# Performance work log

Hardware: AMD Instinct MI355X
Metric: run time of the kernel (lower is better)

## Reference

```python
import jax, jax.numpy as jnp
import numpy as np
import math

N_HEAD = 16

def setup_inputs() -> dict:
    key = jax.random.key(0)
    k1, k2, k3, k4, k5 = jax.random.split(key, 5)
    B, S, D = 2, 2048, 1024
    return {
        "hidden_states": jax.random.normal(k1, (B, S, D), dtype=jnp.float32),
        "c_attn_w": jax.random.normal(k2, (D, 3 * D), dtype=jnp.float32) * 0.02,
        "c_attn_b": jax.random.normal(k3, (3 * D,), dtype=jnp.float32) * 0.02,
        "c_proj_w": jax.random.normal(k4, (D, D), dtype=jnp.float32) * 0.02,
        "c_proj_b": jax.random.normal(k5, (D,), dtype=jnp.float32) * 0.02,
    }

def reference(hidden_states, c_attn_w, c_attn_b, c_proj_w, c_proj_b):
    B, S, D = hidden_states.shape
    H = N_HEAD
    hd = D // H
    # GPT-2 Conv1D: x @ W + b, W is [in, out]
    qkv = hidden_states @ c_attn_w + c_attn_b            # [B,S,3D]
    q, k, v = jnp.split(qkv, 3, axis=-1)                 # each [B,S,D]
    # sparsify_q/k/v_fn are identity hooks in this config
    def to_heads(x):
        return x.reshape(B, S, H, hd).transpose(0, 2, 1, 3)  # [B,H,S,hd]
    q, k, v = to_heads(q), to_heads(k), to_heads(v)
    scores = jnp.einsum("bhqd,bhkd->bhqk", q, k) / math.sqrt(hd)  # [B,H,S,S]
    causal = jnp.triu(jnp.ones((S, S), dtype=bool), k=1)
    scores = jnp.where(causal, jnp.finfo(scores.dtype).min, scores)
    attn = jax.nn.softmax(scores, axis=-1)
    out = jnp.einsum("bhqk,bhkd->bhqd", attn, v)         # [B,H,S,hd]
    out = out.transpose(0, 2, 1, 3).reshape(B, S, D)
    return out @ c_proj_w + c_proj_b
```

## Files before the change

### kernel.cpp

```cpp
#include <hip/hip_runtime.h>
#include <stdint.h>


#define B_   2
#define S_   2048
#define D_   1024
#define H_   16
#define HD_  64

typedef __bf16 bf16x8 __attribute__((ext_vector_type(8)));
typedef float  f32x4  __attribute__((ext_vector_type(4)));
typedef float  f32x16 __attribute__((ext_vector_type(16)));
typedef uint32_t u32x4 __attribute__((ext_vector_type(4)));

__device__ __forceinline__ float b2f(uint16_t u) {
    union { uint32_t i; float f; } x; x.i = ((uint32_t)u) << 16; return x.f;
}
__device__ __forceinline__ uint16_t f2b(float f) {
    uint32_t x = __builtin_bit_cast(uint32_t, f);
    x += 0x7fffu + ((x >> 16) & 1u);
    return (uint16_t)(x >> 16);
}
__device__ __forceinline__ float sq(float f) {
    return fminf(fmaxf(f, -1e4f), 1e4f);
}
__device__ __forceinline__ void async16(const void* g, void* l) {
    __builtin_amdgcn_global_load_lds(
        (const __attribute__((address_space(1))) void*)g,
        (__attribute__((address_space(3))) void*)l, 16, 0, 0);
}

__global__ __launch_bounds__(64)
void kcode(uint16_t* out, float v) { if (threadIdx.x == 0) out[0] = f2b(v); }

__device__ __forceinline__ void cvt4(const float* __restrict__ in,
                                     uint16_t* __restrict__ out, int i) {
    float4 v = *(const float4*)(in + i);
    ushort4 o;
    o.x = f2b(v.x); o.y = f2b(v.y); o.z = f2b(v.z); o.w = f2b(v.w);
    *(ushort4*)(out + i) = o;
}

__device__ __forceinline__ void trans_body(const float* __restrict__ in,
                                           uint16_t* __restrict__ out,
                                           int rows, int cols, int bxx, int byy,
                                           int tid, uint16_t (*tile)[68]) {
    const int tx = tid & 15, ty = tid >> 4;
    const int c0 = bxx * 64, r0 = byy * 64;
#pragma unroll
    for (int p = 0; p < 4; ++p) {
        int rr = ty + p * 16;
        float4 v = *(const float4*)(in + (size_t)(r0 + rr) * cols + c0 + tx * 4);
        tile[rr][tx * 4 + 0] = f2b(v.x);
        tile[rr][tx * 4 + 1] = f2b(v.y);
        tile[rr][tx * 4 + 2] = f2b(v.z);
        tile[rr][tx * 4 + 3] = f2b(v.w);
    }
    __syncthreads();
#pragma unroll
    for (int p = 0; p < 4; ++p) {
        int rr = ty + p * 16;
        ushort4 v;
        v.x = tile[tx * 4 + 0][rr];
        v.y = tile[tx * 4 + 1][rr];
        v.z = tile[tx * 4 + 2][rr];
        v.w = tile[tx * 4 + 3][rr];
        *(ushort4*)(out + (size_t)(c0 + rr) * rows + r0 + tx * 4) = v;
    }
}

__global__ __launch_bounds__(256)
void kprep(const float* __restrict__ hid, const float* __restrict__ ab,
           const float* __restrict__ pb, const float* __restrict__ wA,
           const float* __restrict__ wP, uint16_t* __restrict__ HO,
           uint16_t* __restrict__ bA, uint16_t* __restrict__ bP,
           uint16_t* __restrict__ WtA, uint16_t* __restrict__ WtP) {
    __shared__ __attribute__((aligned(16))) uint16_t tile[64][68];
    const int bx = (int)blockIdx.x, tid = threadIdx.x;
    if (bx < 4096) {
        cvt4(hid, HO, (bx * 256 + tid) * 4);
    } else if (bx < 4100) {
        int i = ((bx - 4096) * 256 + tid) * 4;
        const float* src = (i < 3072) ? ab + i : pb + (i - 3072);
        uint16_t*   dst = (i < 3072) ? bA + i : bP + (i - 3072);
        float4 v = *(const float4*)src;
        ushort4 o;
        o.x = f2b(v.x); o.y = f2b(v.y); o.z = f2b(v.z); o.w = f2b(v.w);
        *(ushort4*)dst = o;
    } else if (bx < 4868) {
        int bb = bx - 4100;
        trans_body(wA, WtA, 1024, 3072, bb % 48, bb / 48, tid, tile);
    } else {
        int bb = bx - 4868;
        trans_body(wP, WtP, 1024, 1024, bb % 16, bb / 16, tid, tile);
    }
}

__global__ __launch_bounds__(256, 2)
void kgemm_qkv(const uint16_t* __restrict__ A, const uint16_t* __restrict__ Bt,
               const uint16_t* __restrict__ bias,
               uint16_t* __restrict__ Qb, uint16_t* __restrict__ Kb,
               uint16_t* __restrict__ Vt) {
    constexpr int KD = 1024;
    __shared__ __attribute__((aligned(16))) uint16_t smem[2][8192];
    const int tid = threadIdx.x, lane = tid & 63, wid = tid >> 6;
    const int r = lane & 15, qd = lane >> 4;
    const int bm = blockIdx.x * 128, bn = blockIdx.y * 128;
    const int wm = (wid & 1) * 64, wn = (wid >> 1) * 64;
    const int sel = (int)blockIdx.y >> 3;
    f32x4 acc[4][4] = {};

    auto stage = [&](int k0, int buf) {
        uint16_t* As = smem[buf];
        uint16_t* Bs = smem[buf] + 4096;
#pragma unroll
        for (int half = 0; half < 2; ++half) {
            int s = half * 256 + tid;
            int row = s >> 2;
            int kq = (s & 3) ^ (row & 3);
            async16(A  + (size_t)(bm + row) * KD + k0 + kq * 8, As + s * 8);
            async16(Bt + (size_t)(bn + row) * KD + k0 + kq * 8, Bs + s * 8);
        }
    };

    stage(0, 0);

    if (sel != 2) {
        for (int t = 0; t < 32; ++t) {
            __syncthreads();
            if (t + 1 < 32) stage((t + 1) * 32, (t + 1) & 1);
            const uint16_t* As = smem[t & 1];
            const uint16_t* Bs = smem[t & 1] + 4096;
            bf16x8 af[4], bfr[4];
#pragma unroll
            for (int i = 0; i < 4; ++i) {
                int ra = wm + i * 16 + r;
                af[i]  = *(const bf16x8*)(As + ((ra * 4) + (qd ^ (ra & 3))) * 8);
                int rb = wn + i * 16 + r;
                bfr[i] = *(const bf16x8*)(Bs + ((rb * 4) + (qd ^ (rb & 3))) * 8);
            }
#pragma unroll
            for (int i = 0; i < 4; ++i)
#pragma unroll
                for (int j = 0; j < 4; ++j)
                    acc[i][j] = __builtin_amdgcn_mfma_f32_16x16x32_bf16(
                        bfr[j], af[i], acc[i][j], 0, 0, 0);
        }
        const float SCq = 0.1803368801111204f;
        uint16_t* dst = sel ? Kb : Qb;
#pragma unroll
        for (int j = 0; j < 4; ++j) {
            int n0 = bn + wn + j * 16 + qd * 4;
            ushort4 b4 = *(const ushort4*)(bias + n0);
            float bv0 = b2f(b4.x), bv1 = b2f(b4.y),
                  bv2 = b2f(b4.z), bv3 = b2f(b4.w);
            int d = n0 & 1023, h = d >> 6, e0 = d & 63;
#pragma unroll
            for (int i = 0; i < 4; ++i) {
                int m = bm + wm + i * 16 + r;
                int bb = m >> 11, s = m & 2047;
                float v0 = acc[i][j][0] + bv0, v1 = acc[i][j][1] + bv1,
                      v2 = acc[i][j][2] + bv2, v3 = acc[i][j][3] + bv3;
                if (sel == 0) { v0 *= SCq; v1 *= SCq; v2 *= SCq; v3 *= SCq; }
                ushort4 o;
                o.x = f2b(sq(v0)); o.y = f2b(sq(v1));
                o.z = f2b(sq(v2)); o.w = f2b(sq(v3));
                *(ushort4*)(dst + (((size_t)bb * H_ + h) * S_ + s) * HD_ + e0) = o;
            }
        }
    } else {
        for (int t = 0; t < 32; ++t) {
            __syncthreads();
            if (t + 1 < 32) stage((t + 1) * 32, (t + 1) & 1);
            const uint16_t* As = smem[t & 1];
            const uint16_t* Bs = smem[t & 1] + 4096;
            bf16x8 af[4], bfr[4];
#pragma unroll
            for (int i = 0; i < 4; ++i) {
                int ra = wm + i * 16 + r;
                af[i]  = *(const bf16x8*)(As + ((ra * 4) + (qd ^ (ra & 3))) * 8);
                int rb = wn + i * 16 + r;
                bfr[i] = *(const bf16x8*)(Bs + ((rb * 4) + (qd ^ (rb & 3))) * 8);
            }
#pragma unroll
            for (int i = 0; i < 4; ++i)
#pragma unroll
                for (int j = 0; j < 4; ++j)
                    acc[i][j] = __builtin_amdgcn_mfma_f32_16x16x32_bf16(
                        af[i], bfr[j], acc[i][j], 0, 0, 0);
        }
#pragma unroll
        for (int j = 0; j < 4; ++j) {
            int n = bn + wn + j * 16 + r;
            float bv = b2f(bias[n]);
            int d = n & 1023, h = d >> 6, e = d & 63;
#pragma unroll
            for (int i = 0; i < 4; ++i) {
                int m0 = bm + wm + i * 16 + qd * 4;
                int bb = m0 >> 11, s0 = m0 & 2047;
                ushort4 o;
                o.x = f2b(sq(acc[i][j][0] + bv));
                o.y = f2b(sq(acc[i][j][1] + bv));
                o.z = f2b(sq(acc[i][j][2] + bv));
                o.w = f2b(sq(acc[i][j][3] + bv));
                *(ushort4*)(Vt + (((size_t)bb * H_ + h) * HD_ + e) * S_ + s0) = o;
            }
        }
    }
}

__global__ __launch_bounds__(256, 2)
void kgemm_proj(const uint16_t* __restrict__ A, const uint16_t* __restrict__ Bt,
                const uint16_t* __restrict__ bias, float* __restrict__ out) {
    constexpr int KD = 1024;
    __shared__ __attribute__((aligned(16))) uint16_t smem[2][6144];
    const int tid = threadIdx.x, lane = tid & 63, wid = tid >> 6;
    const int r = lane & 15, qd = lane >> 4;
    const int bm = blockIdx.x * 64, bn = blockIdx.y * 128;
    const int wm = (wid & 1) * 32, wn = (wid >> 1) * 64;
    f32x4 acc[2][4] = {};

    auto stage = [&](int k0, int buf) {
        uint16_t* As = smem[buf];
        uint16_t* Bs = smem[buf] + 2048;
        {
            int s = tid;
            int row = s >> 2;
            int kq = (s & 3) ^ (row & 3);
            async16(A + (size_t)(bm + row) * KD + k0 + kq * 8, As + s * 8);
        }
#pragma unroll
        for (int half = 0; half < 2; ++half) {
            int s = half * 256 + tid;
            int row = s >> 2;
            int kq = (s & 3) ^ (row & 3);
            async16(Bt + (size_t)(bn + row) * KD + k0 + kq * 8, Bs + s * 8);
        }
    };

    stage(0, 0);

    for (int t = 0; t < 32; ++t) {
        __syncthreads();
        if (t + 1 < 32) stage((t + 1) * 32, (t + 1) & 1);
        const uint16_t* As = smem[t & 1];
        const uint16_t* Bs = smem[t & 1] + 2048;
        bf16x8 af[2], bfr[4];
#pragma unroll
        for (int i = 0; i < 2; ++i) {
            int ra = wm + i * 16 + r;
            af[i] = *(const bf16x8*)(As + ((ra * 4) + (qd ^ (ra & 3))) * 8);
        }
#pragma unroll
        for (int j = 0; j < 4; ++j) {
            int rb = wn + j * 16 + r;
            bfr[j] = *(const bf16x8*)(Bs + ((rb * 4) + (qd ^ (rb & 3))) * 8);
        }
#pragma unroll
        for (int i = 0; i < 2; ++i)
#pragma unroll
            for (int j = 0; j < 4; ++j)
                acc[i][j] = __builtin_amdgcn_mfma_f32_16x16x32_bf16(
                    bfr[j], af[i], acc[i][j], 0, 0, 0);
    }

#pragma unroll
    for (int i = 0; i < 2; ++i) {
        int m = bm + wm + i * 16 + r;
#pragma unroll
        for (int j = 0; j < 4; ++j) {
            int n0 = bn + wn + j * 16 + qd * 4;
            ushort4 b4 = *(const ushort4*)(bias + n0);
            float4 o;
            o.x = sq(acc[i][j][0] + b2f(b4.x));
            o.y = sq(acc[i][j][1] + b2f(b4.y));
            o.z = sq(acc[i][j][2] + b2f(b4.z));
            o.w = sq(acc[i][j][3] + b2f(b4.w));
            *(float4*)(out + (size_t)m * 1024 + n0) = o;
        }
    }
}

__global__ __launch_bounds__(256, 4)
void kattn(const uint16_t* __restrict__ Q, const uint16_t* __restrict__ K,
           const uint16_t* __restrict__ Vt, uint16_t* __restrict__ O) {
    const int d_  = (int)blockIdx.y * 32 + (int)blockIdx.x;
    const int bh  = (d_ & 7) + 8 * ((d_ >> 3) & 3);
    const int qt  = 31 - (d_ >> 5);
    const int tid = threadIdx.x, lane = tid & 63, wid = tid >> 6;
    const int c = lane & 31, hh = lane >> 5;
    const int wq = wid >> 1, wk = wid & 1;
    const uint16_t* Qb = Q  + (size_t)bh * S_ * HD_;
    const int b = bh >> 4, h = bh & 15;

    __shared__ __attribute__((aligned(16))) uint16_t smem[4][4096];
    __shared__ float lsx[4][64];

    const int T = qt + 1;

    const int sA = tid, sB = 256 + tid;
    const int krA = sA >> 3, kcA = (sA & 7) ^ (krA & 7);
    const int krB = sB >> 3, kcB = (sB & 7) ^ (krB & 7);
    const uint16_t* ksA = K  + (size_t)bh * S_ * HD_ + (size_t)krA * HD_ + kcA * 8;
    const uint16_t* ksB = K  + (size_t)bh * S_ * HD_ + (size_t)krB * HD_ + kcB * 8;
    const uint16_t* vsA = Vt + (size_t)bh * HD_ * S_ + (size_t)krA * S_ + kcA * 8;
    const uint16_t* vsB = Vt + (size_t)bh * HD_ * S_ + (size_t)krB * S_ + kcB * 8;

    auto stageto = [&](int buf) {
        async16(ksA, &smem[buf][sA * 8]);
        async16(ksB, &smem[buf][sB * 8]);
        async16(vsA, &smem[2 + buf][sA * 8]);
        async16(vsB, &smem[2 + buf][sB * 8]);
        ksA += 64 * HD_; ksB += 64 * HD_;
        vsA += 64;       vsB += 64;
    };

    stageto(0);

    const int q0 = qt * 64;
    const int qg = q0 + wq * 32 + c;
    bf16x8 qf[4];
#pragma unroll
    for (int cc = 0; cc < 4; ++cc)
        qf[cc] = *(const bf16x8*)(Qb + (size_t)qg * HD_ + cc * 16 + hh * 8);

    const int krow = wk * 32 + c;
    const int kofs0 = krow * 64 + (((0 + hh) ^ (krow & 7)) * 8);
    const int kofs1 = krow * 64 + (((2 + hh) ^ (krow & 7)) * 8);
    const int kofs2 = krow * 64 + (((4 + hh) ^ (krow & 7)) * 8);
    const int kofs3 = krow * 64 + (((6 + hh) ^ (krow & 7)) * 8);
    const int vgA = ((4 * wk + 0 + hh) ^ (c & 7)) * 8;
    const int vgB = ((4 * wk + 2 + hh) ^ (c & 7)) * 8;
    const int vofs00 = c * 64 + vgA,        vofs01 = c * 64 + vgB;
    const int vofs10 = (32 + c) * 64 + vgA, vofs11 = (32 + c) * 64 + vgB;

    const f32x16 ZERO = {};
    f32x16 oacc0 = {}, oacc1 = {};
    float lsum = 0.f;

    auto iter = [&](int buf, int t, bool pf) {
        __syncthreads();
        if (pf) stageto(buf ^ 1);

        const uint16_t* Kc = smem[buf];
        const uint16_t* Vc = smem[2 + buf];

        __builtin_amdgcn_s_setprio(1);
        bf16x8 kf0 = *(const bf16x8*)(Kc + kofs0);
        bf16x8 kf1 = *(const bf16x8*)(Kc + kofs1);
        bf16x8 kf2 = *(const bf16x8*)(Kc + kofs2);
        bf16x8 kf3 = *(const bf16x8*)(Kc + kofs3);
        f32x16 sacc;
        sacc = __builtin_amdgcn_mfma_f32_32x32x16_bf16(kf0, qf[0], ZERO, 0, 0, 0);
        sacc = __builtin_amdgcn_mfma_f32_32x32x16_bf16(kf1, qf[1], sacc, 0, 0, 0);
        sacc = __builtin_amdgcn_mfma_f32_32x32x16_bf16(kf2, qf[2], sacc, 0, 0, 0);
        sacc = __builtin_amdgcn_mfma_f32_32x32x16_bf16(kf3, qf[3], sacc, 0, 0, 0);
        __builtin_amdgcn_s_setprio(0);

        if (t == T - 1) {
            const int kvb = t * 64 + wk * 32 + 4 * hh;
#pragma unroll
            for (int r = 0; r < 16; ++r) {
                int kvgl = kvb + (r & 3) + 8 * (r >> 2);
                if (kvgl > qg) sacc[r] = -3e38f;
            }
        }

        float p[16];
#pragma unroll
        for (int r = 0; r < 16; ++r)
            p[r] = exp2f(fminf(sacc[r], 20.f));
#pragma unroll
        for (int r = 0; r < 16; r += 4)
            lsum += ((p[r] + p[r + 1]) + (p[r + 2] + p[r + 3]));

        uint32_t D[8];
#pragma unroll
        for (int m = 0; m < 8; ++m)
            asm("v_cvt_pk_bf16_f32 %0, %1, %2"
                : "=v"(D[m]) : "v"(p[2 * m]), "v"(p[2 * m + 1]));
        asm("v_permlane32_swap_b32 %0, %1" : "+v"(D[0]), "+v"(D[2]));
        asm("v_permlane32_swap_b32 %0, %1" : "+v"(D[1]), "+v"(D[3]));
        asm("v_permlane32_swap_b32 %0, %1" : "+v"(D[4]), "+v"(D[6]));
        asm("v_permlane32_swap_b32 %0, %1" : "+v"(D[5]), "+v"(D[7]));
        u32x4 w0, w1;
        w0[0] = D[0]; w0[1] = D[1]; w0[2] = D[2]; w0[3] = D[3];
        w1[0] = D[4]; w1[1] = D[5]; w1[2] = D[6]; w1[3] = D[7];
        bf16x8 pf0 = __builtin_bit_cast(bf16x8, w0);
        bf16x8 pf1 = __builtin_bit_cast(bf16x8, w1);

        __builtin_amdgcn_s_setprio(1);
        bf16x8 v00 = *(const bf16x8*)(Vc + vofs00);
        bf16x8 v10 = *(const bf16x8*)(Vc + vofs01);
        bf16x8 v01 = *(const bf16x8*)(Vc + vofs10);
        bf16x8 v11 = *(const bf16x8*)(Vc + vofs11);
        oacc0 = __builtin_amdgcn_mfma_f32_32x32x16_bf16(pf0, v00, oacc0, 0, 0, 0);
        oacc0 = __builtin_amdgcn_mfma_f32_32x32x16_bf16(pf1, v10, oacc0, 0, 0, 0);
        oacc1 = __builtin_amdgcn_mfma_f32_32x32x16_bf16(pf0, v01, oacc1, 0, 0, 0);
        oacc1 = __builtin_amdgcn_mfma_f32_32x32x16_bf16(pf1, v11, oacc1, 0, 0, 0);
        __builtin_amdgcn_s_setprio(0);
    };

    int t = 0;
    while (t + 2 <= T) {
        iter(0, t, true);
        iter(1, t + 1, t + 2 < T);
        t += 2;
    }
    if (t < T) iter(0, t, false);

    lsum += __shfl_xor(lsum, 32);
    __syncthreads();
    float* xch = (float*)&smem[0][0];
    float* myA = xch + wid * 2048;
#pragma unroll
    for (int s = 0; s < 4; ++s) {
        f32x4 a0, a1;
#pragma unroll
        for (int g = 0; g < 4; ++g) { a0[g] = oacc0[4 * s + g]; a1[g] = oacc1[4 * s + g]; }
        *(f32x4*)(myA + 0 * 1024 + s * 256 + lane * 4) = a0;
        *(f32x4*)(myA + 1 * 1024 + s * 256 + lane * 4) = a1;
    }
    lsx[wid][lane] = lsum;
    __syncthreads();
    const int pwid = wid ^ 1;
    float lfull = lsum + lsx[pwid][lane];
    float osum[16];
#pragma unroll
    for (int s = 0; s < 4; ++s) {
        f32x4 po = *(const f32x4*)(xch + pwid * 2048 + wk * 1024 + s * 256 + lane * 4);
#pragma unroll
        for (int g = 0; g < 4; ++g)
            osum[4 * s + g] = (wk ? oacc1[4 * s + g] : oacc0[4 * s + g]) + po[g];
    }
#pragma unroll
    for (int r = 0; r < 16; ++r) {
        int qp = (r & 3) + 8 * (r >> 2) + 4 * hh;
        float inv = 1.0f / __shfl(lfull, qp);
        int qglob = q0 + wq * 32 + qp;
        int hd = wk * 32 + c;
        O[((size_t)b * S_ + qglob) * D_ + h * HD_ + hd] = f2b(sq(osum[r] * inv));
    }
}

extern "C" void kernel_launch(void* const* d_in, const int* in_sizes, int n_in,
                              void* d_out, int out_size, void* d_ws, size_t ws_size,
                              hipStream_t stream) {
    uint16_t* ws = (uint16_t*)d_ws;

    const int exp_sizes[5] = {4194304, 3145728, 3072, 1048576, 1024};
    if (n_in != 5) { kcode<<<1, 64, 0, stream>>>((uint16_t*)d_out, 2950.f); return; }
    for (int i = 0; i < 5; ++i)
        if (in_sizes[i] != exp_sizes[i]) {
            kcode<<<1, 64, 0, stream>>>((uint16_t*)d_out, 3000.f + 100.f * i); return;
        }
    if (out_size != 4194304) { kcode<<<1, 64, 0, stream>>>((uint16_t*)d_out, 2900.f); return; }

    uint16_t* WtA = ws;
    uint16_t* WtP = WtA + 3145728;
    uint16_t* bA  = WtP + 1048576;
    uint16_t* bP  = bA  + 4096;
    uint16_t* Qb  = bP  + 4096;
    uint16_t* Kb  = Qb  + 4194304;
    uint16_t* Vt  = Kb  + 4194304;
    uint16_t* HO  = Vt  + 4194304;
    const size_t NEED = (size_t)((HO + 4194304) - ws) * 2 + 16;
    if (ws_size < NEED) {
        kcode<<<1, 64, 0, stream>>>((uint16_t*)d_out, 1000.f + (float)(ws_size >> 20));
        return;
    }

    kprep<<<5124, 256, 0, stream>>>((const float*)d_in[0], (const float*)d_in[2],
                                    (const float*)d_in[4], (const float*)d_in[1],
                                    (const float*)d_in[3], HO, bA, bP, WtA, WtP);

    kgemm_qkv<<<dim3(32, 24), 256, 0, stream>>>(HO, WtA, bA, Qb, Kb, Vt);
    kattn<<<dim3(32, 32), 256, 0, stream>>>(Qb, Kb, Vt, HO);
    kgemm_proj<<<dim3(64, 8), 256, 0, stream>>>(HO, WtP, bP, (float*)d_out);
}
```

Baseline: 174.9 us.

## Double attention KV tile to 128 keys with 8 waves per block

The attention kernel now uses 512 threads (8 waves) and stages 128 keys per iteration instead of 64, splitting the key dimension across four waves per query half. The cross-wave reduction of partial outputs and row sums is reworked to sum over four waves, and the V shared-memory layout and swizzle are widened to 128 columns. The aim is to halve the number of loop iterations and barriers and to give more MFMA work per sync. In exchange it doubles shared memory per block, which may cut occupancy. The causal mask now covers a 128-key block, so more work on the diagonal tile is masked out and wasted.

```diff
diff --git a/kernel.cpp b/kernel.cpp
--- a/kernel.cpp
+++ b/kernel.cpp
@@ -281,7 +281,7 @@
     }
 }
 
-__global__ __launch_bounds__(256, 4)
+__global__ __launch_bounds__(512, 4)
 void kattn(const uint16_t* __restrict__ Q, const uint16_t* __restrict__ K,
            const uint16_t* __restrict__ Vt, uint16_t* __restrict__ O) {
     const int d_  = (int)blockIdx.y * 32 + (int)blockIdx.x;
@@ -289,30 +289,32 @@
     const int qt  = 31 - (d_ >> 5);
     const int tid = threadIdx.x, lane = tid & 63, wid = tid >> 6;
     const int c = lane & 31, hh = lane >> 5;
-    const int wq = wid >> 1, wk = wid & 1;
-    const uint16_t* Qb = Q  + (size_t)bh * S_ * HD_;
+    const int wq = wid >> 2, wk = wid & 3;
+    const uint16_t* Qb = Q + (size_t)bh * S_ * HD_;
     const int b = bh >> 4, h = bh & 15;
 
-    __shared__ __attribute__((aligned(16))) uint16_t smem[4][4096];
-    __shared__ float lsx[4][64];
-
-    const int T = qt + 1;
-
-    const int sA = tid, sB = 256 + tid;
+    __shared__ __attribute__((aligned(16))) uint16_t smem[4][8192];
+    __shared__ float lsx[8][64];
+
+    const int T = (qt + 2) >> 1;
+
+    const int sA = tid, sB = 512 + tid;
     const int krA = sA >> 3, kcA = (sA & 7) ^ (krA & 7);
     const int krB = sB >> 3, kcB = (sB & 7) ^ (krB & 7);
+    const int vrA = sA >> 4, vcA = (sA & 15) ^ (vrA & 15);
+    const int vrB = sB >> 4, vcB = (sB & 15) ^ (vrB & 15);
     const uint16_t* ksA = K  + (size_t)bh * S_ * HD_ + (size_t)krA * HD_ + kcA * 8;
     const uint16_t* ksB = K  + (size_t)bh * S_ * HD_ + (size_t)krB * HD_ + kcB * 8;
-    const uint16_t* vsA = Vt + (size_t)bh * HD_ * S_ + (size_t)krA * S_ + kcA * 8;
-    const uint16_t* vsB = Vt + (size_t)bh * HD_ * S_ + (size_t)krB * S_ + kcB * 8;
+    const uint16_t* vsA = Vt + (size_t)bh * HD_ * S_ + (size_t)vrA * S_ + vcA * 8;
+    const uint16_t* vsB = Vt + (size_t)bh * HD_ * S_ + (size_t)vrB * S_ + vcB * 8;
 
     auto stageto = [&](int buf) {
         async16(ksA, &smem[buf][sA * 8]);
         async16(ksB, &smem[buf][sB * 8]);
         async16(vsA, &smem[2 + buf][sA * 8]);
         async16(vsB, &smem[2 + buf][sB * 8]);
-        ksA += 64 * HD_; ksB += 64 * HD_;
-        vsA += 64;       vsB += 64;
+        ksA += 128 * HD_; ksB += 128 * HD_;
+        vsA += 128;       vsB += 128;
     };
 
     stageto(0);
@@ -329,10 +331,10 @@
     const int kofs1 = krow * 64 + (((2 + hh) ^ (krow & 7)) * 8);
     const int kofs2 = krow * 64 + (((4 + hh) ^ (krow & 7)) * 8);
     const int kofs3 = krow * 64 + (((6 + hh) ^ (krow & 7)) * 8);
-    const int vgA = ((4 * wk + 0 + hh) ^ (c & 7)) * 8;
-    const int vgB = ((4 * wk + 2 + hh) ^ (c & 7)) * 8;
-    const int vofs00 = c * 64 + vgA,        vofs01 = c * 64 + vgB;
-    const int vofs10 = (32 + c) * 64 + vgA, vofs11 = (32 + c) * 64 + vgB;
+    const int vofs00 = c * 128 +        (((4 * wk + 0 + hh) ^ (c & 15)) * 8);
+    const int vofs01 = c * 128 +        (((4 * wk + 2 + hh) ^ (c & 15)) * 8);
+    const int vofs10 = (32 + c) * 128 + (((4 * wk + 0 + hh) ^ ((32 + c) & 15)) * 8);
+    const int vofs11 = (32 + c) * 128 + (((4 * wk + 2 + hh) ^ ((32 + c) & 15)) * 8);
 
     const f32x16 ZERO = {};
     f32x16 oacc0 = {}, oacc1 = {};
@@ -358,7 +360,7 @@
         __builtin_amdgcn_s_setprio(0);
 
         if (t == T - 1) {
-            const int kvb = t * 64 + wk * 32 + 4 * hh;
+            const int kvb = t * 128 + wk * 32 + 4 * hh;
 #pragma unroll
             for (int r = 0; r < 16; ++r) {
                 int kvgl = kvb + (r & 3) + 8 * (r >> 2);
@@ -418,28 +420,37 @@
         f32x4 a0, a1;
 #pragma unroll
         for (int g = 0; g < 4; ++g) { a0[g] = oacc0[4 * s + g]; a1[g] = oacc1[4 * s + g]; }
-        *(f32x4*)(myA + 0 * 1024 + s * 256 + lane * 4) = a0;
-        *(f32x4*)(myA + 1 * 1024 + s * 256 + lane * 4) = a1;
+        *(f32x4*)(myA + (s)*256 + lane * 4) = a0;
+        *(f32x4*)(myA + (4 + s) * 256 + lane * 4) = a1;
     }
     lsx[wid][lane] = lsum;
     __syncthreads();
-    const int pwid = wid ^ 1;
-    float lfull = lsum + lsx[pwid][lane];
-    float osum[16];
-#pragma unroll
-    for (int s = 0; s < 4; ++s) {
-        f32x4 po = *(const f32x4*)(xch + pwid * 2048 + wk * 1024 + s * 256 + lane * 4);
-#pragma unroll
-        for (int g = 0; g < 4; ++g)
-            osum[4 * s + g] = (wk ? oacc1[4 * s + g] : oacc0[4 * s + g]) + po[g];
-    }
-#pragma unroll
-    for (int r = 0; r < 16; ++r) {
-        int qp = (r & 3) + 8 * (r >> 2) + 4 * hh;
+    float lfull = 0.f;
+#pragma unroll
+    for (int w = 0; w < 4; ++w) lfull += lsx[wq * 4 + w][lane];
+    float osum[8];
+#pragma unroll
+    for (int i = 0; i < 8; i += 4) {
+        int s = 2 * wk + (i >> 2);
+        f32x4 acc4 = {};
+#pragma unroll
+        for (int w = 0; w < 4; ++w) {
+            f32x4 po = *(const f32x4*)(xch + (wq * 4 + w) * 2048 + s * 256 + lane * 4);
+#pragma unroll
+            for (int g = 0; g < 4; ++g) acc4[g] += po[g];
+        }
+#pragma unroll
+        for (int g = 0; g < 4; ++g) osum[i + g] = acc4[g];
+    }
+#pragma unroll
+    for (int i = 0; i < 8; ++i) {
+        int R = 8 * wk + i;
+        int half = R >> 4, rr = R & 15;
+        int qp = (rr & 3) + 8 * (rr >> 2) + 4 * hh;
         float inv = 1.0f / __shfl(lfull, qp);
         int qglob = q0 + wq * 32 + qp;
-        int hd = wk * 32 + c;
-        O[((size_t)b * S_ + qglob) * D_ + h * HD_ + hd] = f2b(sq(osum[r] * inv));
+        int hd = half * 32 + c;
+        O[((size_t)b * S_ + qglob) * D_ + h * HD_ + hd] = f2b(sq(osum[i] * inv));
     }
 }
 
@@ -475,6 +486,6 @@
                                     (const float*)d_in[3], HO, bA, bP, WtA, WtP);
 
     kgemm_qkv<<<dim3(32, 24), 256, 0, stream>>>(HO, WtA, bA, Qb, Kb, Vt);
-    kattn<<<dim3(32, 32), 256, 0, stream>>>(Qb, Kb, Vt, HO);
+    kattn<<<dim3(32, 32), 512, 0, stream>>>(Qb, Kb, Vt, HO);
     kgemm_proj<<<dim3(64, 8), 256, 0, stream>>>(HO, WtP, bP, (float*)d_out);
 }
```

After: 174.1 us. Within noise of the previous version (-0.5%).

## Double GEMM K-step per barrier and remap blocks for XCD-aware L2 locality

Applied to the files above, without the earlier changes.

Both the QKV and output-projection GEMMs now stage two 32-wide K slices per pipeline step (64 per sync), halving the number of barriers and loop iterations at the cost of doubled shared memory per block. Block indices are also remapped so that consecutive hardware-dispatched blocks (interleaved across 8 XCDs) land on neighboring output tiles, aiming to improve L2 reuse of A/B panels. The attention kernel's V offset expression is rewritten equivalently. Larger LDS may reduce occupancy for the 2-blocks-per-CU launch bounds.

```diff
diff --git a/kernel.cpp b/kernel.cpp
--- a/kernel.cpp
+++ b/kernel.cpp
@@ -102,49 +102,58 @@
                uint16_t* __restrict__ Qb, uint16_t* __restrict__ Kb,
                uint16_t* __restrict__ Vt) {
     constexpr int KD = 1024;
-    __shared__ __attribute__((aligned(16))) uint16_t smem[2][8192];
+    __shared__ __attribute__((aligned(16))) uint16_t smem[2][16384];
     const int tid = threadIdx.x, lane = tid & 63, wid = tid >> 6;
     const int r = lane & 15, qd = lane >> 4;
-    const int bm = blockIdx.x * 128, bn = blockIdx.y * 128;
+    const int idw = (int)blockIdx.y * 32 + (int)blockIdx.x;
+    const int nid = (idw & 7) * 96 + (idw >> 3);
+    const int bm = (nid & 31) * 128, bn = (nid >> 5) * 128;
     const int wm = (wid & 1) * 64, wn = (wid >> 1) * 64;
-    const int sel = (int)blockIdx.y >> 3;
+    const int sel = nid >> 8;
     f32x4 acc[4][4] = {};
 
     auto stage = [&](int k0, int buf) {
         uint16_t* As = smem[buf];
-        uint16_t* Bs = smem[buf] + 4096;
-#pragma unroll
-        for (int half = 0; half < 2; ++half) {
-            int s = half * 256 + tid;
-            int row = s >> 2;
-            int kq = (s & 3) ^ (row & 3);
-            async16(A  + (size_t)(bm + row) * KD + k0 + kq * 8, As + s * 8);
-            async16(Bt + (size_t)(bn + row) * KD + k0 + kq * 8, Bs + s * 8);
-        }
+        uint16_t* Bs = smem[buf] + 8192;
+#pragma unroll
+        for (int hh = 0; hh < 2; ++hh)
+#pragma unroll
+            for (int half = 0; half < 2; ++half) {
+                int s = half * 256 + tid;
+                int row = s >> 2;
+                int kq = (s & 3) ^ (row & 3);
+                async16(A  + (size_t)(bm + row) * KD + k0 + hh * 32 + kq * 8,
+                        As + hh * 4096 + s * 8);
+                async16(Bt + (size_t)(bn + row) * KD + k0 + hh * 32 + kq * 8,
+                        Bs + hh * 4096 + s * 8);
+            }
     };
 
     stage(0, 0);
 
     if (sel != 2) {
-        for (int t = 0; t < 32; ++t) {
+        for (int t = 0; t < 16; ++t) {
             __syncthreads();
-            if (t + 1 < 32) stage((t + 1) * 32, (t + 1) & 1);
-            const uint16_t* As = smem[t & 1];
-            const uint16_t* Bs = smem[t & 1] + 4096;
-            bf16x8 af[4], bfr[4];
-#pragma unroll
-            for (int i = 0; i < 4; ++i) {
-                int ra = wm + i * 16 + r;
-                af[i]  = *(const bf16x8*)(As + ((ra * 4) + (qd ^ (ra & 3))) * 8);
-                int rb = wn + i * 16 + r;
-                bfr[i] = *(const bf16x8*)(Bs + ((rb * 4) + (qd ^ (rb & 3))) * 8);
-            }
-#pragma unroll
-            for (int i = 0; i < 4; ++i)
-#pragma unroll
-                for (int j = 0; j < 4; ++j)
-                    acc[i][j] = __builtin_amdgcn_mfma_f32_16x16x32_bf16(
-                        bfr[j], af[i], acc[i][j], 0, 0, 0);
+            if (t + 1 < 16) stage((t + 1) * 64, (t + 1) & 1);
+#pragma unroll
+            for (int hh = 0; hh < 2; ++hh) {
+                const uint16_t* As = smem[t & 1] + hh * 4096;
+                const uint16_t* Bs = smem[t & 1] + 8192 + hh * 4096;
+                bf16x8 af[4], bfr[4];
+#pragma unroll
+                for (int i = 0; i < 4; ++i) {
+                    int ra = wm + i * 16 + r;
+                    af[i]  = *(const bf16x8*)(As + ((ra * 4) + (qd ^ (ra & 3))) * 8);
+                    int rb = wn + i * 16 + r;
+                    bfr[i] = *(const bf16x8*)(Bs + ((rb * 4) + (qd ^ (rb & 3))) * 8);
+                }
+#pragma unroll
+                for (int i = 0; i < 4; ++i)
+#pragma unroll
+                    for (int j = 0; j < 4; ++j)
+                        acc[i][j] = __builtin_amdgcn_mfma_f32_16x16x32_bf16(
+                            bfr[j], af[i], acc[i][j], 0, 0, 0);
+            }
         }
         const float SCq = 0.1803368801111204f;
         uint16_t* dst = sel ? Kb : Qb;
@@ -169,25 +178,28 @@
             }
         }
     } else {
-        for (int t = 0; t < 32; ++t) {
+        for (int t = 0; t < 16; ++t) {
             __syncthreads();
-            if (t + 1 < 32) stage((t + 1) * 32, (t + 1) & 1);
-            const uint16_t* As = smem[t & 1];
-            const uint16_t* Bs = smem[t & 1] + 4096;
-            bf16x8 af[4], bfr[4];
-#pragma unroll
-            for (int i = 0; i < 4; ++i) {
-                int ra = wm + i * 16 + r;
-                af[i]  = *(const bf16x8*)(As + ((ra * 4) + (qd ^ (ra & 3))) * 8);
-                int rb = wn + i * 16 + r;
-                bfr[i] = *(const bf16x8*)(Bs + ((rb * 4) + (qd ^ (rb & 3))) * 8);
-            }
-#pragma unroll
-            for (int i = 0; i < 4; ++i)
-#pragma unroll
-                for (int j = 0; j < 4; ++j)
-                    acc[i][j] = __builtin_amdgcn_mfma_f32_16x16x32_bf16(
-                        af[i], bfr[j], acc[i][j], 0, 0, 0);
+            if (t + 1 < 16) stage((t + 1) * 64, (t + 1) & 1);
+#pragma unroll
+            for (int hh = 0; hh < 2; ++hh) {
+                const uint16_t* As = smem[t & 1] + hh * 4096;
+                const uint16_t* Bs = smem[t & 1] + 8192 + hh * 4096;
+                bf16x8 af[4], bfr[4];
+#pragma unroll
+                for (int i = 0; i < 4; ++i) {
+                    int ra = wm + i * 16 + r;
+                    af[i]  = *(const bf16x8*)(As + ((ra * 4) + (qd ^ (ra & 3))) * 8);
+                    int rb = wn + i * 16 + r;
+                    bfr[i] = *(const bf16x8*)(Bs + ((rb * 4) + (qd ^ (rb & 3))) * 8);
+                }
+#pragma unroll
+                for (int i = 0; i < 4; ++i)
+#pragma unroll
+                    for (int j = 0; j < 4; ++j)
+                        acc[i][j] = __builtin_amdgcn_mfma_f32_16x16x32_bf16(
+                            af[i], bfr[j], acc[i][j], 0, 0, 0);
+            }
         }
 #pragma unroll
         for (int j = 0; j < 4; ++j) {
@@ -213,55 +225,65 @@
 void kgemm_proj(const uint16_t* __restrict__ A, const uint16_t* __restrict__ Bt,
                 const uint16_t* __restrict__ bias, float* __restrict__ out) {
     constexpr int KD = 1024;
-    __shared__ __attribute__((aligned(16))) uint16_t smem[2][6144];
+    __shared__ __attribute__((aligned(16))) uint16_t smem[2][12288];
     const int tid = threadIdx.x, lane = tid & 63, wid = tid >> 6;
     const int r = lane & 15, qd = lane >> 4;
-    const int bm = blockIdx.x * 64, bn = blockIdx.y * 128;
+    const int idw = (int)blockIdx.y * 64 + (int)blockIdx.x;
+    const int nid = (idw & 7) * 64 + (idw >> 3);
+    const int bm = (nid & 63) * 64, bn = (nid >> 6) * 128;
     const int wm = (wid & 1) * 32, wn = (wid >> 1) * 64;
     f32x4 acc[2][4] = {};
 
     auto stage = [&](int k0, int buf) {
         uint16_t* As = smem[buf];
-        uint16_t* Bs = smem[buf] + 2048;
-        {
-            int s = tid;
-            int row = s >> 2;
-            int kq = (s & 3) ^ (row & 3);
-            async16(A + (size_t)(bm + row) * KD + k0 + kq * 8, As + s * 8);
-        }
-#pragma unroll
-        for (int half = 0; half < 2; ++half) {
-            int s = half * 256 + tid;
-            int row = s >> 2;
-            int kq = (s & 3) ^ (row & 3);
-            async16(Bt + (size_t)(bn + row) * KD + k0 + kq * 8, Bs + s * 8);
+        uint16_t* Bs = smem[buf] + 4096;
+#pragma unroll
+        for (int hh = 0; hh < 2; ++hh) {
+            {
+                int s = tid;
+                int row = s >> 2;
+                int kq = (s & 3) ^ (row & 3);
+                async16(A + (size_t)(bm + row) * KD + k0 + hh * 32 + kq * 8,
+                        As + hh * 2048 + s * 8);
+            }
+#pragma unroll
+            for (int half = 0; half < 2; ++half) {
+                int s = half * 256 + tid;
+                int row = s >> 2;
+                int kq = (s & 3) ^ (row & 3);
+                async16(Bt + (size_t)(bn + row) * KD + k0 + hh * 32 + kq * 8,
+                        Bs + hh * 4096 + s * 8);
+            }
         }
     };
 
     stage(0, 0);
 
-    for (int t = 0; t < 32; ++t) {
+    for (int t = 0; t < 16; ++t) {
         __syncthreads();
-        if (t + 1 < 32) stage((t + 1) * 32, (t + 1) & 1);
-        const uint16_t* As = smem[t & 1];
-        const uint16_t* Bs = smem[t & 1] + 2048;
-        bf16x8 af[2], bfr[4];
-#pragma unroll
-        for (int i = 0; i < 2; ++i) {
-            int ra = wm + i * 16 + r;
-            af[i] = *(const bf16x8*)(As + ((ra * 4) + (qd ^ (ra & 3))) * 8);
-        }
-#pragma unroll
-        for (int j = 0; j < 4; ++j) {
-            int rb = wn + j * 16 + r;
-            bfr[j] = *(const bf16x8*)(Bs + ((rb * 4) + (qd ^ (rb & 3))) * 8);
-        }
-#pragma unroll
-        for (int i = 0; i < 2; ++i)
-#pragma unroll
-            for (int j = 0; j < 4; ++j)
-                acc[i][j] = __builtin_amdgcn_mfma_f32_16x16x32_bf16(
-                    bfr[j], af[i], acc[i][j], 0, 0, 0);
+        if (t + 1 < 16) stage((t + 1) * 64, (t + 1) & 1);
+#pragma unroll
+        for (int hh = 0; hh < 2; ++hh) {
+            const uint16_t* As = smem[t & 1] + hh * 2048;
+            const uint16_t* Bs = smem[t & 1] + 4096 + hh * 4096;
+            bf16x8 af[2], bfr[4];
+#pragma unroll
+            for (int i = 0; i < 2; ++i) {
+                int ra = wm + i * 16 + r;
+                af[i] = *(const bf16x8*)(As + ((ra * 4) + (qd ^ (ra & 3))) * 8);
+            }
+#pragma unroll
+            for (int j = 0; j < 4; ++j) {
+                int rb = wn + j * 16 + r;
+                bfr[j] = *(const bf16x8*)(Bs + ((rb * 4) + (qd ^ (rb & 3))) * 8);
+            }
+#pragma unroll
+            for (int i = 0; i < 2; ++i)
+#pragma unroll
+                for (int j = 0; j < 4; ++j)
+                    acc[i][j] = __builtin_amdgcn_mfma_f32_16x16x32_bf16(
+                        bfr[j], af[i], acc[i][j], 0, 0, 0);
+        }
     }
 
 #pragma unroll
@@ -290,7 +312,7 @@
     const int tid = threadIdx.x, lane = tid & 63, wid = tid >> 6;
     const int c = lane & 31, hh = lane >> 5;
     const int wq = wid >> 1, wk = wid & 1;
-    const uint16_t* Qb = Q  + (size_t)bh * S_ * HD_;
+    const uint16_t* Qb = Q + (size_t)bh * S_ * HD_;
     const int b = bh >> 4, h = bh & 15;
 
     __shared__ __attribute__((aligned(16))) uint16_t smem[4][4096];
@@ -332,7 +354,8 @@
     const int vgA = ((4 * wk + 0 + hh) ^ (c & 7)) * 8;
     const int vgB = ((4 * wk + 2 + hh) ^ (c & 7)) * 8;
     const int vofs00 = c * 64 + vgA,        vofs01 = c * 64 + vgB;
-    const int vofs10 = (32 + c) * 64 + vgA, vofs11 = (32 + c) * 64 + vgB;
+    const int vofs10 = (32 + c) * 64 + (((4 * wk + 0 + hh) ^ ((32 + c) & 7)) * 8);
+    const int vofs11 = (32 + c) * 64 + (((4 * wk + 2 + hh) ^ ((32 + c) & 7)) * 8);
 
     const f32x16 ZERO = {};
     f32x16 oacc0 = {}, oacc1 = {};
```

After: 178.2 us. No clear change (+1.9%).
